# Optimization experiments

Measured on AMD Instinct MI355X. Metric: run time of the kernel, lower is better.

## Reference

```python
import jax, jax.numpy as jnp
import numpy as np

N_NODES = 100000
N_EDGES = 1600000
IN_CH = 128


def _sage_conv(x, src, dst, Wl, b, Wr, n_nodes):
    # PyG SAGEConv (aggr='mean', root_weight=True):
    #   out_i = lin_l(mean_{j->i} x_j) + lin_r(x_i)
    msg = x[src]                                             # [E, F]
    agg = jax.ops.segment_sum(msg, dst, num_segments=n_nodes)  # [N, F]
    deg = jax.ops.segment_sum(jnp.ones((src.shape[0],), x.dtype), dst,
                              num_segments=n_nodes)          # [N]
    mean = agg / jnp.maximum(deg, 1.0)[:, None]
    return mean @ Wl + b + x @ Wr


def setup_inputs() -> dict:
    key = jax.random.key(0)
    ks = jax.random.split(key, 10)
    x = jax.random.normal(ks[0], (N_NODES, IN_CH), dtype=jnp.float32)
    edge_index = jax.random.randint(ks[1], (2, N_EDGES), 0, N_NODES, dtype=jnp.int64)
    s = 0.05
    return {
        "x": x,
        "edge_index": edge_index,
        "W1l": jax.random.normal(ks[2], (IN_CH, 32), dtype=jnp.float32) * s,
        "b1": jax.random.normal(ks[3], (32,), dtype=jnp.float32) * s,
        "W1r": jax.random.normal(ks[4], (IN_CH, 32), dtype=jnp.float32) * s,
        "W2l": jax.random.normal(ks[5], (32, 16), dtype=jnp.float32) * s,
        "b2": jax.random.normal(ks[6], (16,), dtype=jnp.float32) * s,
        "W2r": jax.random.normal(ks[7], (32, 16), dtype=jnp.float32) * s,
        "Wfc": jax.random.normal(ks[8], (16, 2), dtype=jnp.float32) * s,
        "bfc": jax.random.normal(ks[9], (2,), dtype=jnp.float32) * s,
    }


def reference(x, edge_index, W1l, b1, W1r, W2l, b2, W2r, Wfc, bfc):
    src, dst = edge_index[0], edge_index[1]
    n = x.shape[0]
    h = jax.nn.relu(_sage_conv(x, src, dst, W1l, b1, W1r, n))   # [N, 32]
    h = jax.nn.relu(_sage_conv(h, src, dst, W2l, b2, W2r, n))   # [N, 16]
    return h @ Wfc + bfc                                        # [N, 2]
```

## Files before the change

kernel.cpp:

```cpp
#include <hip/hip_runtime.h>

#define TPB 256
#define BK_SHIFT 7
#define BK_SIZE 128
#define NBK_MAX 784
#define EPT 32
#define CAP 2816

typedef __attribute__((ext_vector_type(8))) short bf16x8;
typedef __attribute__((ext_vector_type(4))) float f32x4;
typedef __attribute__((ext_vector_type(2))) float f32x2;
typedef __attribute__((ext_vector_type(4))) unsigned short u16x4;

__device__ __forceinline__ unsigned short f2bf(float f) {
    unsigned u = __float_as_uint(f);
    unsigned r = (u + 0x7FFFu + ((u >> 16) & 1u)) >> 16;
    return (unsigned short)r;
}
__device__ __forceinline__ float bf2f(unsigned short b) {
    return __uint_as_float((unsigned)b << 16);
}
__device__ __forceinline__ void acc4(f32x4& a, u16x4 v) {
    a.x += bf2f(v.x); a.y += bf2f(v.y); a.z += bf2f(v.z); a.w += bf2f(v.w);
}

__global__ __launch_bounds__(256) void bin_scatter(
    const int* __restrict__ src, const int* __restrict__ dst,
    int* __restrict__ gfill, int* __restrict__ pk, int E, int NBK)
{
    __shared__ int lcnt[NBK_MAX];
    __shared__ int lbase[NBK_MAX];
    __shared__ int lrank[NBK_MAX];
    const int t = threadIdx.x;
    const int e0 = blockIdx.x * (256 * EPT);

    for (int i = t; i < NBK; i += 256) { lcnt[i] = 0; lrank[i] = 0; }
    __syncthreads();

    int dreg[EPT];
    #pragma unroll 4
    for (int k = 0; k < EPT; ++k) {
        int e = e0 + k * 256 + t;
        dreg[k] = (e < E) ? __builtin_nontemporal_load(&dst[e]) : -1;
        if (dreg[k] >= 0) atomicAdd(&lcnt[dreg[k] >> BK_SHIFT], 1);
    }
    __syncthreads();

    for (int i = t; i < NBK; i += 256) {
        int c = lcnt[i];
        if (c) lbase[i] = atomicAdd(&gfill[i], c);
    }
    __syncthreads();

    #pragma unroll 4
    for (int k = 0; k < EPT; ++k) {
        int e = e0 + k * 256 + t;
        if (e < E) {
            int d = dreg[k];
            int s = __builtin_nontemporal_load(&src[e]);
            int b = d >> BK_SHIFT;
            int r = atomicAdd(&lrank[b], 1);
            int pos = lbase[b] + r;
            if (pos < CAP)
                pk[(size_t)b * CAP + pos] = (s << BK_SHIFT) | (d & (BK_SIZE - 1));
        }
    }
}

__global__ __launch_bounds__(256) void gemm1_mfma(
    const float* __restrict__ A,
    const float* __restrict__ Wl,
    const float* __restrict__ Wr,
    const float* __restrict__ b,
    unsigned short* __restrict__ Yb,
    float* __restrict__ C,
    int N)
{
    const int lane = threadIdx.x & 63;
    const int m    = lane & 15;
    const int quad = lane >> 4;
    const int wave   = blockIdx.x * (blockDim.x >> 6) + (threadIdx.x >> 6);
    const int nwaves = gridDim.x * (blockDim.x >> 6);
    const int ntiles = (N + 15) >> 4;

    bf16x8 Bf[4][4];
    #pragma unroll
    for (int kc = 0; kc < 4; ++kc) {
        #pragma unroll
        for (int jt = 0; jt < 4; ++jt) {
            const float* W = (jt < 2) ? Wl : Wr;
            const int col = (jt & 1) * 16 + m;
            #pragma unroll
            for (int j = 0; j < 8; ++j) {
                int k = kc * 32 + quad * 8 + j;
                Bf[kc][jt][j] = (short)f2bf(W[k * 32 + col]);
            }
        }
    }

    const float bias0 = b[m];
    const float bias1 = b[16 + m];

    for (int tile = wave; tile < ntiles; tile += nwaves) {
        const int node0 = tile * 16;
        const int gn = node0 + m;
        const bool okA = gn < N;
        const float* rowp = A + (size_t)gn * 128;

        bf16x8 Af[4];
        #pragma unroll
        for (int kc = 0; kc < 4; ++kc) {
            f32x4 v0 = {0.f, 0.f, 0.f, 0.f};
            f32x4 v1 = {0.f, 0.f, 0.f, 0.f};
            if (okA) {
                v0 = __builtin_nontemporal_load((const f32x4*)&rowp[kc * 32 + quad * 8]);
                v1 = __builtin_nontemporal_load((const f32x4*)&rowp[kc * 32 + quad * 8 + 4]);
            }
            Af[kc][0] = (short)f2bf(v0.x); Af[kc][1] = (short)f2bf(v0.y);
            Af[kc][2] = (short)f2bf(v0.z); Af[kc][3] = (short)f2bf(v0.w);
            Af[kc][4] = (short)f2bf(v1.x); Af[kc][5] = (short)f2bf(v1.y);
            Af[kc][6] = (short)f2bf(v1.z); Af[kc][7] = (short)f2bf(v1.w);
        }

        f32x4 acc[4] = {{0.f,0.f,0.f,0.f},{0.f,0.f,0.f,0.f},
                        {0.f,0.f,0.f,0.f},{0.f,0.f,0.f,0.f}};
        #pragma unroll
        for (int kc = 0; kc < 4; ++kc) {
            #pragma unroll
            for (int jt = 0; jt < 4; ++jt)
                acc[jt] = __builtin_amdgcn_mfma_f32_16x16x32_bf16(
                    Af[kc], Bf[kc][jt], acc[jt], 0, 0, 0);
        }

        const int nodeBase = node0 + quad * 4;
        #pragma unroll
        for (int reg = 0; reg < 4; ++reg) {
            const int node = nodeBase + reg;
            if (node < N) {
                Yb[(size_t)node * 32 + m]      = f2bf(acc[0][reg]);
                Yb[(size_t)node * 32 + 16 + m] = f2bf(acc[1][reg]);
                C [(size_t)node * 32 + m]      = acc[2][reg] + bias0;
                C [(size_t)node * 32 + 16 + m] = acc[3][reg] + bias1;
            }
        }
    }
}

__global__ __launch_bounds__(256) void gather_gemm2(
    const int* __restrict__ gfill, const int* __restrict__ pk,
    const unsigned short* __restrict__ Yb,
    const float* __restrict__ c1,
    const float* __restrict__ W2l, const float* __restrict__ W2r,
    const float* __restrict__ b2,
    unsigned short* __restrict__ y2b, float* __restrict__ c2, int N)
{
    __shared__ int lcnt[BK_SIZE];
    __shared__ int soff[BK_SIZE];
    __shared__ int wcur[BK_SIZE];
    __shared__ int sidx[CAP];

    const int t = threadIdx.x;
    const int b = blockIdx.x;
    const size_t base = (size_t)b * CAP;
    const int cnt  = min(gfill[b], CAP);
    const int node0 = b * BK_SIZE;

    if (t < BK_SIZE) lcnt[t] = 0;
    __syncthreads();

    for (int j = t; j < cnt; j += 256)
        atomicAdd(&lcnt[__builtin_nontemporal_load(&pk[base + j]) & (BK_SIZE - 1)], 1);
    __syncthreads();

    int v = (t < BK_SIZE) ? lcnt[t] : 0;
    if (t < BK_SIZE) soff[t] = v;
    __syncthreads();
    for (int off = 1; off < BK_SIZE; off <<= 1) {
        int u = (t < BK_SIZE && t >= off) ? soff[t - off] : 0;
        __syncthreads();
        if (t < BK_SIZE) soff[t] += u;
        __syncthreads();
    }
    if (t < BK_SIZE) wcur[t] = soff[t] - v;
    __syncthreads();

    for (int j = t; j < cnt; j += 256) {
        int pv = pk[base + j];
        int d  = pv & (BK_SIZE - 1);
        int pos = atomicAdd(&wcur[d], 1);
        sidx[pos] = pv >> BK_SHIFT;
    }
    __syncthreads();

    const int q = t & 7;
    #pragma unroll
    for (int pass = 0; pass < 4; ++pass) {
        const int nl = pass * 32 + (t >> 3);
        const int node = node0 + nl;
        const bool active = node < N;
        float h[4] = {0.f, 0.f, 0.f, 0.f};
        if (active) {
            const int deg = lcnt[nl];
            const int en  = soff[nl];
            const int st  = en - deg;
            const float w = 1.0f / fmaxf((float)deg, 1.0f);

            f32x4 a0 = {0.f,0.f,0.f,0.f};
            f32x4 a1 = {0.f,0.f,0.f,0.f};
            f32x4 a2 = {0.f,0.f,0.f,0.f};
            f32x4 a3 = {0.f,0.f,0.f,0.f};
            int j = st;
            for (; j + 3 < en; j += 4) {
                int s0 = sidx[j], s1 = sidx[j+1], s2 = sidx[j+2], s3 = sidx[j+3];
                u16x4 v0 = *(const u16x4*)&Yb[(size_t)s0 * 32 + q * 4];
                u16x4 v1 = *(const u16x4*)&Yb[(size_t)s1 * 32 + q * 4];
                u16x4 v2 = *(const u16x4*)&Yb[(size_t)s2 * 32 + q * 4];
                u16x4 v3 = *(const u16x4*)&Yb[(size_t)s3 * 32 + q * 4];
                acc4(a0, v0); acc4(a1, v1); acc4(a2, v2); acc4(a3, v3);
            }
            for (; j < en; ++j) {
                u16x4 vv = *(const u16x4*)&Yb[(size_t)sidx[j] * 32 + q * 4];
                acc4(a0, vv);
            }
            f32x4 acc;
            acc.x = (a0.x + a1.x) + (a2.x + a3.x);
            acc.y = (a0.y + a1.y) + (a2.y + a3.y);
            acc.z = (a0.z + a1.z) + (a2.z + a3.z);
            acc.w = (a0.w + a1.w) + (a2.w + a3.w);

            f32x4 c = __builtin_nontemporal_load((const f32x4*)&c1[(size_t)node * 32 + q * 4]);
            h[0] = fmaxf(c.x + acc.x * w, 0.f);
            h[1] = fmaxf(c.y + acc.y * w, 0.f);
            h[2] = fmaxf(c.z + acc.z * w, 0.f);
            h[3] = fmaxf(c.w + acc.w * w, 0.f);
        }

        const int  j0  = q * 4;
        const bool isY = (j0 < 16);
        const int  jj  = isY ? j0 : (j0 - 16);
        const float* Wb = isY ? W2l : W2r;

        float o0 = 0.f, o1 = 0.f, o2 = 0.f, o3 = 0.f;
        #pragma unroll
        for (int k = 0; k < 32; ++k) {
            float hk = __shfl(h[k & 3], k >> 2, 8);
            f32x4 wv = *(const f32x4*)&Wb[k * 16 + jj];
            o0 += hk * wv.x; o1 += hk * wv.y; o2 += hk * wv.z; o3 += hk * wv.w;
        }

        if (active) {
            if (isY) {
                u16x4 r;
                r.x = f2bf(o0); r.y = f2bf(o1); r.z = f2bf(o2); r.w = f2bf(o3);
                *(u16x4*)&y2b[(size_t)node * 16 + jj] = r;
            } else {
                f32x4 bb = *(const f32x4*)&b2[jj];
                f32x4 ov = {o0 + bb.x, o1 + bb.y, o2 + bb.z, o3 + bb.w};
                __builtin_nontemporal_store(ov, (f32x4*)&c2[(size_t)node * 16 + jj]);
            }
        }
    }
}

__global__ __launch_bounds__(256) void gather_final(
    const int* __restrict__ gfill, const int* __restrict__ pk,
    const unsigned short* __restrict__ Yb,
    const float* __restrict__ c2,
    const float* __restrict__ Wfc,
    const float* __restrict__ bfc,
    float* __restrict__ out, int N)
{
    __shared__ int lcnt[BK_SIZE];
    __shared__ int soff[BK_SIZE];
    __shared__ int wcur[BK_SIZE];
    __shared__ int sidx[CAP];

    const int t = threadIdx.x;
    const int b = blockIdx.x;
    const size_t base = (size_t)b * CAP;
    const int cnt  = min(gfill[b], CAP);
    const int node0 = b * BK_SIZE;

    if (t < BK_SIZE) lcnt[t] = 0;
    __syncthreads();

    for (int j = t; j < cnt; j += 256)
        atomicAdd(&lcnt[__builtin_nontemporal_load(&pk[base + j]) & (BK_SIZE - 1)], 1);
    __syncthreads();

    int v = (t < BK_SIZE) ? lcnt[t] : 0;
    if (t < BK_SIZE) soff[t] = v;
    __syncthreads();
    for (int off = 1; off < BK_SIZE; off <<= 1) {
        int u = (t < BK_SIZE && t >= off) ? soff[t - off] : 0;
        __syncthreads();
        if (t < BK_SIZE) soff[t] += u;
        __syncthreads();
    }
    if (t < BK_SIZE) wcur[t] = soff[t] - v;
    __syncthreads();

    for (int j = t; j < cnt; j += 256) {
        int pv = pk[base + j];
        int d  = pv & (BK_SIZE - 1);
        int pos = atomicAdd(&wcur[d], 1);
        sidx[pos] = pv >> BK_SHIFT;
    }
    __syncthreads();

    const int q = t & 3;
    #pragma unroll
    for (int pass = 0; pass < 2; ++pass) {
        const int nl = pass * 64 + (t >> 2);
        const int node = node0 + nl;
        if (node < N) {
            const int deg = lcnt[nl];
            const int en  = soff[nl];
            const int st  = en - deg;
            const float w = 1.0f / fmaxf((float)deg, 1.0f);

            f32x4 a0 = {0.f,0.f,0.f,0.f};
            f32x4 a1 = {0.f,0.f,0.f,0.f};
            f32x4 a2 = {0.f,0.f,0.f,0.f};
            f32x4 a3 = {0.f,0.f,0.f,0.f};
            int j = st;
            for (; j + 3 < en; j += 4) {
                int s0 = sidx[j], s1 = sidx[j+1], s2 = sidx[j+2], s3 = sidx[j+3];
                u16x4 v0 = *(const u16x4*)&Yb[(size_t)s0 * 16 + q * 4];
                u16x4 v1 = *(const u16x4*)&Yb[(size_t)s1 * 16 + q * 4];
                u16x4 v2 = *(const u16x4*)&Yb[(size_t)s2 * 16 + q * 4];
                u16x4 v3 = *(const u16x4*)&Yb[(size_t)s3 * 16 + q * 4];
                acc4(a0, v0); acc4(a1, v1); acc4(a2, v2); acc4(a3, v3);
            }
            for (; j < en; ++j) {
                u16x4 vv = *(const u16x4*)&Yb[(size_t)sidx[j] * 16 + q * 4];
                acc4(a0, vv);
            }
            f32x4 acc;
            acc.x = (a0.x + a1.x) + (a2.x + a3.x);
            acc.y = (a0.y + a1.y) + (a2.y + a3.y);
            acc.z = (a0.z + a1.z) + (a2.z + a3.z);
            acc.w = (a0.w + a1.w) + (a2.w + a3.w);

            f32x4 c = __builtin_nontemporal_load((const f32x4*)&c2[(size_t)node * 16 + q * 4]);
            float h0 = fmaxf(c.x + acc.x * w, 0.f);
            float h1 = fmaxf(c.y + acc.y * w, 0.f);
            float h2 = fmaxf(c.z + acc.z * w, 0.f);
            float h3 = fmaxf(c.w + acc.w * w, 0.f);

            const float* Wq = &Wfc[q * 8];
            float o0 = h0 * Wq[0] + h1 * Wq[2] + h2 * Wq[4] + h3 * Wq[6];
            float o1 = h0 * Wq[1] + h1 * Wq[3] + h2 * Wq[5] + h3 * Wq[7];

            o0 += __shfl_xor(o0, 1); o0 += __shfl_xor(o0, 2);
            o1 += __shfl_xor(o1, 1); o1 += __shfl_xor(o1, 2);

            if (q == 0) {
                f32x2 ov = {o0 + bfc[0], o1 + bfc[1]};
                __builtin_nontemporal_store(ov, (f32x2*)&out[(size_t)node * 2]);
            }
        } else {
            float z = 0.f;
            z += __shfl_xor(z, 1); z += __shfl_xor(z, 2);
        }
    }
}

extern "C" void kernel_launch(void* const* d_in, const int* in_sizes, int n_in,
                              void* d_out, int out_size, void* d_ws, size_t ws_size,
                              hipStream_t stream)
{
    const float* x   = (const float*)d_in[0];
    const int*   ei  = (const int*)d_in[1];
    const float* W1l = (const float*)d_in[2];
    const float* b1  = (const float*)d_in[3];
    const float* W1r = (const float*)d_in[4];
    const float* W2l = (const float*)d_in[5];
    const float* b2  = (const float*)d_in[6];
    const float* W2r = (const float*)d_in[7];
    const float* Wfc = (const float*)d_in[8];
    const float* bfc = (const float*)d_in[9];
    float* out = (float*)d_out;

    const int N = in_sizes[0] / 128;
    const int E = in_sizes[1] / 2;
    const int* src = ei;
    const int* dst = ei + E;

    const int NBK = (N + BK_SIZE - 1) / BK_SIZE;

    int*   gfill = (int*)d_ws;
    int*   pk    = gfill + NBK_MAX;
    unsigned short* y1b = (unsigned short*)(pk + (size_t)NBK_MAX * CAP);
    float* c1          = (float*)(y1b + (size_t)N * 32);
    unsigned short* y2b = (unsigned short*)(c1 + (size_t)N * 32);
    float* c2          = (float*)(y2b + (size_t)N * 16);

    hipMemsetAsync(gfill, 0, (size_t)NBK_MAX * sizeof(int), stream);
    {
        int nb = (E + 256 * EPT - 1) / (256 * EPT);
        bin_scatter<<<nb, 256, 0, stream>>>(src, dst, gfill, pk, E, NBK);
    }

    gemm1_mfma<<<1024, TPB, 0, stream>>>(x, W1l, W1r, b1, y1b, c1, N);

    gather_gemm2<<<NBK, TPB, 0, stream>>>(
        gfill, pk, y1b, c1, W2l, W2r, b2, y2b, c2, N);

    gather_final<<<NBK, TPB, 0, stream>>>(
        gfill, pk, y2b, c2, Wfc, bfc, out, N);
}
```

Measured before the change: 229.8 us.

## Merge edge binning and first GEMM into one horizontally fused launch

Folds the bin_scatter kernel and the gemm1 MFMA kernel into a single launch, where the first NSC blocks bin edges and the rest run the layer-1 GEMM. The two independent phases can then overlap on the GPU and one kernel launch goes away. The scatter now reads dst/src as int4 vectors instead of holding 32 per-thread registers, and non-temporal loads of pk in the gather kernels become normal loads. The risks are higher shared-memory and register use for the GEMM blocks, which may lower their occupancy, and int4 loads that assume E is a multiple of 4.

```diff
diff --git a/kernel.cpp b/kernel.cpp
--- a/kernel.cpp
+++ b/kernel.cpp
@@ -4,8 +4,9 @@
 #define BK_SHIFT 7
 #define BK_SIZE 128
 #define NBK_MAX 784
-#define EPT 32
 #define CAP 2816
+#define SC_EPB 8192
+#define GEMM_BLKS 1024
 
 typedef __attribute__((ext_vector_type(8))) short bf16x8;
 typedef __attribute__((ext_vector_type(4))) float f32x4;
@@ -24,50 +25,9 @@
     a.x += bf2f(v.x); a.y += bf2f(v.y); a.z += bf2f(v.z); a.w += bf2f(v.w);
 }
 
-__global__ __launch_bounds__(256) void bin_scatter(
+__global__ __launch_bounds__(256) void build_and_gemm1(
     const int* __restrict__ src, const int* __restrict__ dst,
-    int* __restrict__ gfill, int* __restrict__ pk, int E, int NBK)
-{
-    __shared__ int lcnt[NBK_MAX];
-    __shared__ int lbase[NBK_MAX];
-    __shared__ int lrank[NBK_MAX];
-    const int t = threadIdx.x;
-    const int e0 = blockIdx.x * (256 * EPT);
-
-    for (int i = t; i < NBK; i += 256) { lcnt[i] = 0; lrank[i] = 0; }
-    __syncthreads();
-
-    int dreg[EPT];
-    #pragma unroll 4
-    for (int k = 0; k < EPT; ++k) {
-        int e = e0 + k * 256 + t;
-        dreg[k] = (e < E) ? __builtin_nontemporal_load(&dst[e]) : -1;
-        if (dreg[k] >= 0) atomicAdd(&lcnt[dreg[k] >> BK_SHIFT], 1);
-    }
-    __syncthreads();
-
-    for (int i = t; i < NBK; i += 256) {
-        int c = lcnt[i];
-        if (c) lbase[i] = atomicAdd(&gfill[i], c);
-    }
-    __syncthreads();
-
-    #pragma unroll 4
-    for (int k = 0; k < EPT; ++k) {
-        int e = e0 + k * 256 + t;
-        if (e < E) {
-            int d = dreg[k];
-            int s = __builtin_nontemporal_load(&src[e]);
-            int b = d >> BK_SHIFT;
-            int r = atomicAdd(&lrank[b], 1);
-            int pos = lbase[b] + r;
-            if (pos < CAP)
-                pk[(size_t)b * CAP + pos] = (s << BK_SHIFT) | (d & (BK_SIZE - 1));
-        }
-    }
-}
-
-__global__ __launch_bounds__(256) void gemm1_mfma(
+    int* __restrict__ gfill, int* __restrict__ pk, int E, int NBK, int NSC,
     const float* __restrict__ A,
     const float* __restrict__ Wl,
     const float* __restrict__ Wr,
@@ -76,11 +36,76 @@
     float* __restrict__ C,
     int N)
 {
+    __shared__ int lcnt[NBK_MAX];
+    __shared__ int lbase[NBK_MAX];
+    __shared__ int lrank[NBK_MAX];
+
+    if ((int)blockIdx.x < NSC) {
+        const int t = threadIdx.x;
+        const int e0 = blockIdx.x * SC_EPB;
+
+        for (int i = t; i < NBK; i += 256) { lcnt[i] = 0; lrank[i] = 0; }
+        __syncthreads();
+
+        #pragma unroll
+        for (int k = 0; k < SC_EPB / 1024; ++k) {
+            int e = e0 + k * 1024 + t * 4;
+            if (e < E) {
+                int4 d = *(const int4*)&dst[e];
+                atomicAdd(&lcnt[d.x >> BK_SHIFT], 1);
+                atomicAdd(&lcnt[d.y >> BK_SHIFT], 1);
+                atomicAdd(&lcnt[d.z >> BK_SHIFT], 1);
+                atomicAdd(&lcnt[d.w >> BK_SHIFT], 1);
+            }
+        }
+        __syncthreads();
+
+        for (int i = t; i < NBK; i += 256) {
+            int c = lcnt[i];
+            if (c) lbase[i] = atomicAdd(&gfill[i], c);
+        }
+        __syncthreads();
+
+        #pragma unroll
+        for (int k = 0; k < SC_EPB / 1024; ++k) {
+            int e = e0 + k * 1024 + t * 4;
+            if (e < E) {
+                int4 d = *(const int4*)&dst[e];
+                int4 s = *(const int4*)&src[e];
+                {
+                    int bb = d.x >> BK_SHIFT;
+                    int pos = lbase[bb] + atomicAdd(&lrank[bb], 1);
+                    if (pos < CAP) pk[(size_t)bb * CAP + pos] =
+                        (s.x << BK_SHIFT) | (d.x & (BK_SIZE - 1));
+                }
+                {
+                    int bb = d.y >> BK_SHIFT;
+                    int pos = lbase[bb] + atomicAdd(&lrank[bb], 1);
+                    if (pos < CAP) pk[(size_t)bb * CAP + pos] =
+                        (s.y << BK_SHIFT) | (d.y & (BK_SIZE - 1));
+                }
+                {
+                    int bb = d.z >> BK_SHIFT;
+                    int pos = lbase[bb] + atomicAdd(&lrank[bb], 1);
+                    if (pos < CAP) pk[(size_t)bb * CAP + pos] =
+                        (s.z << BK_SHIFT) | (d.z & (BK_SIZE - 1));
+                }
+                {
+                    int bb = d.w >> BK_SHIFT;
+                    int pos = lbase[bb] + atomicAdd(&lrank[bb], 1);
+                    if (pos < CAP) pk[(size_t)bb * CAP + pos] =
+                        (s.w << BK_SHIFT) | (d.w & (BK_SIZE - 1));
+                }
+            }
+        }
+        return;
+    }
+
     const int lane = threadIdx.x & 63;
     const int m    = lane & 15;
     const int quad = lane >> 4;
-    const int wave   = blockIdx.x * (blockDim.x >> 6) + (threadIdx.x >> 6);
-    const int nwaves = gridDim.x * (blockDim.x >> 6);
+    const int wave   = (blockIdx.x - NSC) * (blockDim.x >> 6) + (threadIdx.x >> 6);
+    const int nwaves = GEMM_BLKS * (blockDim.x >> 6);
     const int ntiles = (N + 15) >> 4;
 
     bf16x8 Bf[4][4];
@@ -169,7 +194,7 @@
     __syncthreads();
 
     for (int j = t; j < cnt; j += 256)
-        atomicAdd(&lcnt[__builtin_nontemporal_load(&pk[base + j]) & (BK_SIZE - 1)], 1);
+        atomicAdd(&lcnt[pk[base + j] & (BK_SIZE - 1)], 1);
     __syncthreads();
 
     int v = (t < BK_SIZE) ? lcnt[t] : 0;
@@ -285,7 +310,7 @@
     __syncthreads();
 
     for (int j = t; j < cnt; j += 256)
-        atomicAdd(&lcnt[__builtin_nontemporal_load(&pk[base + j]) & (BK_SIZE - 1)], 1);
+        atomicAdd(&lcnt[pk[base + j] & (BK_SIZE - 1)], 1);
     __syncthreads();
 
     int v = (t < BK_SIZE) ? lcnt[t] : 0;
@@ -388,6 +413,7 @@
     const int* dst = ei + E;
 
     const int NBK = (N + BK_SIZE - 1) / BK_SIZE;
+    const int NSC = (E + SC_EPB - 1) / SC_EPB;
 
     int*   gfill = (int*)d_ws;
     int*   pk    = gfill + NBK_MAX;
@@ -397,12 +423,9 @@
     float* c2          = (float*)(y2b + (size_t)N * 16);
 
     hipMemsetAsync(gfill, 0, (size_t)NBK_MAX * sizeof(int), stream);
-    {
-        int nb = (E + 256 * EPT - 1) / (256 * EPT);
-        bin_scatter<<<nb, 256, 0, stream>>>(src, dst, gfill, pk, E, NBK);
-    }
-
-    gemm1_mfma<<<1024, TPB, 0, stream>>>(x, W1l, W1r, b1, y1b, c1, N);
+    build_and_gemm1<<<NSC + GEMM_BLKS, TPB, 0, stream>>>(
+        src, dst, gfill, pk, E, NBK, NSC,
+        x, W1l, W1r, b1, y1b, c1, N);
 
     gather_gemm2<<<NBK, TPB, 0, stream>>>(
         gfill, pk, y1b, c1, W2l, W2r, b2, y2b, c2, N);
```

After: 201.9 us. 12.2% less time.
